# Optimization experiments

Measured on AMD Instinct MI355X. Metric: run time of the kernel, lower is better.

## Reference

```python
import jax, jax.numpy as jnp
import numpy as np

NUM_GRAPHS = 512


def setup_inputs() -> dict:
    key = jax.random.key(0)
    ks = jax.random.split(key, 12)
    N, E, D, H, C = 100000, 1600000, 128, 128, 10
    x = jax.random.normal(ks[0], (N, D), dtype=jnp.float32)
    edge_index = jax.random.randint(ks[1], (2, E), 0, N, dtype=jnp.int64)
    batch = jnp.sort(jax.random.randint(ks[2], (N,), 0, NUM_GRAPHS, dtype=jnp.int64))
    def glorot(k, fan_in, fan_out):
        s = jnp.sqrt(6.0 / (fan_in + fan_out))
        return jax.random.uniform(k, (fan_in, fan_out), jnp.float32, -s, s)
    return {
        "x": x, "edge_index": edge_index, "batch": batch,
        "W_init": glorot(ks[3], D, H), "b_init": jnp.zeros((H,), jnp.float32),
        "W_h0": glorot(ks[4], H, H), "b_h0": jnp.zeros((H,), jnp.float32),
        "W_h1": glorot(ks[5], H, H), "b_h1": jnp.zeros((H,), jnp.float32),
        "W_out": glorot(ks[6], H, C), "b_out": jnp.zeros((C,), jnp.float32),
    }


def reference(x, edge_index, batch, W_init, b_init, W_h0, b_h0, W_h1, b_h1, W_out, b_out):
    N = x.shape[0]
    loop = jnp.arange(N, dtype=edge_index.dtype)
    # add self-loops (PyG GCNConv default)
    row = jnp.concatenate([edge_index[0], loop])  # source
    col = jnp.concatenate([edge_index[1], loop])  # target
    # symmetric normalization D^-1/2 (A+I) D^-1/2, degrees on target index
    deg = jax.ops.segment_sum(jnp.ones_like(col, dtype=x.dtype), col, num_segments=N)
    dis = jnp.where(deg > 0, jax.lax.rsqrt(jnp.maximum(deg, 1e-12)), 0.0)
    norm = dis[row] * dis[col]  # [E+N]

    def gcn_conv(h, W, b):
        h = h @ W                                    # linear first (as in PyG)
        msg = h[row] * norm[:, None]                 # gather + scale
        return jax.ops.segment_sum(msg, col, num_segments=N) + b  # scatter-add

    h = jax.nn.relu(gcn_conv(x, W_init, b_init))
    h = jax.nn.relu(gcn_conv(h, W_h0, b_h0))
    h = jax.nn.relu(gcn_conv(h, W_h1, b_h1))
    h = gcn_conv(h, W_out, b_out)
    # global mean pooling over graphs
    sums = jax.ops.segment_sum(h, batch, num_segments=NUM_GRAPHS)
    cnt = jax.ops.segment_sum(jnp.ones((N, 1), h.dtype), batch, num_segments=NUM_GRAPHS)
    return sums / jnp.maximum(cnt, 1.0)
```

## Files before the change

### kernel.cpp

```cpp
#include <hip/hip_runtime.h>


#define SCAN_BLOCKS 64
#define SCAN_THREADS (SCAN_BLOCKS * 256)

typedef unsigned short u16;
typedef unsigned int   u32;
typedef __attribute__((ext_vector_type(8))) short bf16x8;
typedef __attribute__((ext_vector_type(4))) float f32x4;

static __device__ __forceinline__ u16 f2bf(float x) {
    u32 u = __float_as_uint(x);
    u32 r = (u + 0x7fffu + ((u >> 16) & 1u)) >> 16;
    return (u16)r;
}
static __device__ __forceinline__ float bf_lo(u32 p) { return __uint_as_float(p << 16); }
static __device__ __forceinline__ float bf_hi(u32 p) { return __uint_as_float(p & 0xffff0000u); }

__global__ __launch_bounds__(256) void k_count(const int* __restrict__ col, int E,
                                               int* __restrict__ cnt,
                                               u16* __restrict__ rank) {
    int e = blockIdx.x * 256 + threadIdx.x;
    if (e < E) rank[e] = (u16)atomicAdd(&cnt[col[e]], 1);
}

__global__ __launch_bounds__(256) void k_scan1(const int* __restrict__ cnt,
                                               int* __restrict__ tsum, int N) {
    int t = blockIdx.x * 256 + threadIdx.x;
    int strip = (N + SCAN_THREADS - 1) / SCAN_THREADS;
    int s0 = t * strip;
    int s1 = s0 + strip; if (s1 > N) s1 = N;
    int s = 0;
    for (int i = s0; i < s1; ++i) s += (cnt[i] + 3) & ~3;
    tsum[t] = s;
}

__global__ __launch_bounds__(1024) void k_scan2(int* __restrict__ tsum) {
    __shared__ int part[1024];
    int t = threadIdx.x;
    int base = t * 16;
    int local[16];
    int s = 0;
    #pragma unroll
    for (int i = 0; i < 16; ++i) { local[i] = tsum[base + i]; s += local[i]; }
    part[t] = s;
    __syncthreads();
    for (int off = 1; off < 1024; off <<= 1) {
        int v = part[t];
        int add = (t >= off) ? part[t - off] : 0;
        __syncthreads();
        part[t] = v + add;
        __syncthreads();
    }
    int run = (t == 0) ? 0 : part[t - 1];
    #pragma unroll
    for (int i = 0; i < 16; ++i) { int c = local[i]; tsum[base + i] = run; run += c; }
}

__global__ __launch_bounds__(256) void k_scan3(const int* __restrict__ cnt,
                                               const int* __restrict__ tsum,
                                               int* __restrict__ rowptr,
                                               float* __restrict__ dis,
                                               int* __restrict__ csr, int N) {
    int t = blockIdx.x * 256 + threadIdx.x;
    int strip = (N + SCAN_THREADS - 1) / SCAN_THREADS;
    int s0 = t * strip;
    int s1 = s0 + strip; if (s1 > N) s1 = N;
    int run = tsum[t];
    for (int i = s0; i < s1; ++i) {
        int c = cnt[i];
        int r = (c + 3) & ~3;
        rowptr[i] = run;
        for (int p = run + c; p < run + r; ++p) csr[p] = N;
        run += r;
        dis[i] = rsqrtf((float)(c + 1));
    }
    if (t == SCAN_THREADS - 1) rowptr[N] = run;
}

__global__ __launch_bounds__(256) void k_fill(const int* __restrict__ row,
                                              const int* __restrict__ col, int E,
                                              const int* __restrict__ rowptr,
                                              const u16* __restrict__ rank,
                                              int* __restrict__ csr) {
    int e = blockIdx.x * 256 + threadIdx.x;
    if (e < E) {
        int c = col[e];
        csr[rowptr[c] + (int)rank[e]] = row[e];
    }
}

__global__ __launch_bounds__(256) void k_cast(const float* __restrict__ src,
                                              const float* __restrict__ dis,
                                              u16* __restrict__ bX,
                                              u16* __restrict__ bA,
                                              u16* __restrict__ bB, int N) {
    int i = blockIdx.x * 256 + threadIdx.x;
    int total = (N + 1) * 32;
    if (i >= total) return;
    int v = i >> 5;
    if (v < N) {
        float dv = dis[v];
        float4 val = ((const float4*)src)[i];
        ushort4 o;
        o.x = f2bf(dv * val.x); o.y = f2bf(dv * val.y);
        o.z = f2bf(dv * val.z); o.w = f2bf(dv * val.w);
        ((ushort4*)bX)[i] = o;
    } else {
        ushort4 z = {0, 0, 0, 0};
        ((ushort4*)bX)[i] = z;
        ((ushort4*)bA)[i] = z;
        ((ushort4*)bB)[i] = z;
    }
}

__global__ __launch_bounds__(256) void k_wprep4(const float* __restrict__ W0,
                                                const float* __restrict__ W1,
                                                const float* __restrict__ W2,
                                                const float* __restrict__ Wo,
                                                u32* __restrict__ whi,
                                                u32* __restrict__ wlo, int C) {
    if (blockIdx.x < 24) {
        int which = blockIdx.x >> 3;
        const float* W = (which == 0) ? W0 : (which == 1) ? W1 : W2;
        int t = (blockIdx.x & 7) * 256 + threadIdx.x;
        int lane = t & 63;
        int nk = t >> 6;
        int k0 = nk & 3;
        int ntile = nk >> 2;
        int n = ntile * 16 + (lane & 15);
        int kbase = k0 * 32 + (lane >> 4) * 8;
        u32 hi[4], lo[4];
        #pragma unroll
        for (int tt = 0; tt < 4; ++tt) {
            float w0 = W[(kbase + 2 * tt) * 128 + n];
            float w1 = W[(kbase + 2 * tt + 1) * 128 + n];
            u16 h0 = f2bf(w0), h1 = f2bf(w1);
            u16 l0 = f2bf(w0 - __uint_as_float((u32)h0 << 16));
            u16 l1 = f2bf(w1 - __uint_as_float((u32)h1 << 16));
            hi[tt] = (u32)h0 | ((u32)h1 << 16);
            lo[tt] = (u32)l0 | ((u32)l1 << 16);
        }
        uint4 qh = {hi[0], hi[1], hi[2], hi[3]};
        uint4 ql = {lo[0], lo[1], lo[2], lo[3]};
        int base = which * 2048;
        ((uint4*)whi)[base + t] = qh;
        ((uint4*)wlo)[base + t] = ql;
    } else {
        int t = threadIdx.x;
        int lane = t & 63;
        int k0 = t >> 6;
        int n = lane & 15;
        int kbase = k0 * 32 + (lane >> 4) * 8;
        bool vc = (n < C);
        u32 hi[4], lo[4];
        #pragma unroll
        for (int tt = 0; tt < 4; ++tt) {
            float w0 = vc ? Wo[(kbase + 2 * tt) * C + n] : 0.f;
            float w1 = vc ? Wo[(kbase + 2 * tt + 1) * C + n] : 0.f;
            u16 h0 = f2bf(w0), h1 = f2bf(w1);
            u16 l0 = f2bf(w0 - __uint_as_float((u32)h0 << 16));
            u16 l1 = f2bf(w1 - __uint_as_float((u32)h1 << 16));
            hi[tt] = (u32)h0 | ((u32)h1 << 16);
            lo[tt] = (u32)l0 | ((u32)l1 << 16);
        }
        uint4 qh = {hi[0], hi[1], hi[2], hi[3]};
        uint4 ql = {lo[0], lo[1], lo[2], lo[3]};
        ((uint4*)whi)[6144 + t] = qh;
        ((uint4*)wlo)[6144 + t] = ql;
    }
}

__global__ __launch_bounds__(256) void k_fused(const u16* __restrict__ hin,
                                               const u32* __restrict__ whi,
                                               const u32* __restrict__ wlo,
                                               const float* __restrict__ bias,
                                               u16* __restrict__ hout,
                                               const int* __restrict__ rowptr,
                                               const int* __restrict__ csr,
                                               const float* __restrict__ dis,
                                               int N, int scale_out,
                                               int proj,
                                               const u32* __restrict__ pwhi,
                                               const u32* __restrict__ pwlo,
                                               float* __restrict__ tmpC) {
    __shared__ u32 sS[32 * 68];
    __shared__ float dS[32];
    int tid = threadIdx.x;
    int wave = tid >> 6;
    int lane = tid & 63;
    int row0 = blockIdx.x * 32;
    const u32* hin32 = (const u32*)hin;
    const int4* csr4 = (const int4*)csr;

    for (int j = 0; j < 8; j += 2) {
        int va = row0 + wave * 8 + j;
        int vb = va + 1;
        bool hA = va < N, hB = vb < N;
        float ax = 0.f, ay = 0.f, bx = 0.f, by = 0.f;
        int ia = 0, ea = 0, ib = 0, eb = 0;
        float dva = 1.f, dvb = 1.f;
        if (hA) {
            u32 p = hin32[((u32)va << 6) + lane];
            ax = bf_lo(p); ay = bf_hi(p);
            ia = rowptr[va]; ea = rowptr[va + 1];
            dva = dis[va];
        }
        if (hB) {
            u32 p = hin32[((u32)vb << 6) + lane];
            bx = bf_lo(p); by = bf_hi(p);
            ib = rowptr[vb]; eb = rowptr[vb + 1];
            dvb = dis[vb];
        }
        while ((ia + 8 <= ea) & (ib + 8 <= eb)) {
            int4 a0 = csr4[(u32)ia >> 2];
            int4 a1 = csr4[((u32)ia >> 2) + 1];
            int4 b0 = csr4[(u32)ib >> 2];
            int4 b1 = csr4[((u32)ib >> 2) + 1];
            u32 pa0 = hin32[((u32)a0.x << 6) + lane];
            u32 pa1 = hin32[((u32)a0.y << 6) + lane];
            u32 pa2 = hin32[((u32)a0.z << 6) + lane];
            u32 pa3 = hin32[((u32)a0.w << 6) + lane];
            u32 pa4 = hin32[((u32)a1.x << 6) + lane];
            u32 pa5 = hin32[((u32)a1.y << 6) + lane];
            u32 pa6 = hin32[((u32)a1.z << 6) + lane];
            u32 pa7 = hin32[((u32)a1.w << 6) + lane];
            u32 pb0 = hin32[((u32)b0.x << 6) + lane];
            u32 pb1 = hin32[((u32)b0.y << 6) + lane];
            u32 pb2 = hin32[((u32)b0.z << 6) + lane];
            u32 pb3 = hin32[((u32)b0.w << 6) + lane];
            u32 pb4 = hin32[((u32)b1.x << 6) + lane];
            u32 pb5 = hin32[((u32)b1.y << 6) + lane];
            u32 pb6 = hin32[((u32)b1.z << 6) + lane];
            u32 pb7 = hin32[((u32)b1.w << 6) + lane];
            ax += bf_lo(pa0) + bf_lo(pa1) + bf_lo(pa2) + bf_lo(pa3);
            ay += bf_hi(pa0) + bf_hi(pa1) + bf_hi(pa2) + bf_hi(pa3);
            ax += bf_lo(pa4) + bf_lo(pa5) + bf_lo(pa6) + bf_lo(pa7);
            ay += bf_hi(pa4) + bf_hi(pa5) + bf_hi(pa6) + bf_hi(pa7);
            bx += bf_lo(pb0) + bf_lo(pb1) + bf_lo(pb2) + bf_lo(pb3);
            by += bf_hi(pb0) + bf_hi(pb1) + bf_hi(pb2) + bf_hi(pb3);
            bx += bf_lo(pb4) + bf_lo(pb5) + bf_lo(pb6) + bf_lo(pb7);
            by += bf_hi(pb4) + bf_hi(pb5) + bf_hi(pb6) + bf_hi(pb7);
            ia += 8; ib += 8;
        }
        while (ia + 8 <= ea) {
            int4 a0 = csr4[(u32)ia >> 2];
            int4 a1 = csr4[((u32)ia >> 2) + 1];
            u32 p0 = hin32[((u32)a0.x << 6) + lane];
            u32 p1 = hin32[((u32)a0.y << 6) + lane];
            u32 p2 = hin32[((u32)a0.z << 6) + lane];
            u32 p3 = hin32[((u32)a0.w << 6) + lane];
            u32 p4 = hin32[((u32)a1.x << 6) + lane];
            u32 p5 = hin32[((u32)a1.y << 6) + lane];
            u32 p6 = hin32[((u32)a1.z << 6) + lane];
            u32 p7 = hin32[((u32)a1.w << 6) + lane];
            ax += bf_lo(p0) + bf_lo(p1) + bf_lo(p2) + bf_lo(p3);
            ay += bf_hi(p0) + bf_hi(p1) + bf_hi(p2) + bf_hi(p3);
            ax += bf_lo(p4) + bf_lo(p5) + bf_lo(p6) + bf_lo(p7);
            ay += bf_hi(p4) + bf_hi(p5) + bf_hi(p6) + bf_hi(p7);
            ia += 8;
        }
        if (ia < ea) {
            int4 a0 = csr4[(u32)ia >> 2];
            u32 p0 = hin32[((u32)a0.x << 6) + lane];
            u32 p1 = hin32[((u32)a0.y << 6) + lane];
            u32 p2 = hin32[((u32)a0.z << 6) + lane];
            u32 p3 = hin32[((u32)a0.w << 6) + lane];
            ax += bf_lo(p0) + bf_lo(p1) + bf_lo(p2) + bf_lo(p3);
            ay += bf_hi(p0) + bf_hi(p1) + bf_hi(p2) + bf_hi(p3);
        }
        while (ib + 8 <= eb) {
            int4 b0 = csr4[(u32)ib >> 2];
            int4 b1 = csr4[((u32)ib >> 2) + 1];
            u32 p0 = hin32[((u32)b0.x << 6) + lane];
            u32 p1 = hin32[((u32)b0.y << 6) + lane];
            u32 p2 = hin32[((u32)b0.z << 6) + lane];
            u32 p3 = hin32[((u32)b0.w << 6) + lane];
            u32 p4 = hin32[((u32)b1.x << 6) + lane];
            u32 p5 = hin32[((u32)b1.y << 6) + lane];
            u32 p6 = hin32[((u32)b1.z << 6) + lane];
            u32 p7 = hin32[((u32)b1.w << 6) + lane];
            bx += bf_lo(p0) + bf_lo(p1) + bf_lo(p2) + bf_lo(p3);
            by += bf_hi(p0) + bf_hi(p1) + bf_hi(p2) + bf_hi(p3);
            bx += bf_lo(p4) + bf_lo(p5) + bf_lo(p6) + bf_lo(p7);
            by += bf_hi(p4) + bf_hi(p5) + bf_hi(p6) + bf_hi(p7);
            ib += 8;
        }
        if (ib < eb) {
            int4 b0 = csr4[(u32)ib >> 2];
            u32 p0 = hin32[((u32)b0.x << 6) + lane];
            u32 p1 = hin32[((u32)b0.y << 6) + lane];
            u32 p2 = hin32[((u32)b0.z << 6) + lane];
            u32 p3 = hin32[((u32)b0.w << 6) + lane];
            bx += bf_lo(p0) + bf_lo(p1) + bf_lo(p2) + bf_lo(p3);
            by += bf_hi(p0) + bf_hi(p1) + bf_hi(p2) + bf_hi(p3);
        }
        if (hA) {
            sS[(wave * 8 + j) * 65 + lane] =
                (u32)f2bf(dva * ax) | ((u32)f2bf(dva * ay) << 16);
            if (lane == 0) dS[wave * 8 + j] = dva;
        }
        if (hB) {
            sS[(wave * 8 + j + 1) * 65 + lane] =
                (u32)f2bf(dvb * bx) | ((u32)f2bf(dvb * by) << 16);
            if (lane == 0) dS[wave * 8 + j + 1] = dvb;
        }
    }
    __syncthreads();

    f32x4 acc[2][2] = {{{0.f,0.f,0.f,0.f},{0.f,0.f,0.f,0.f}},
                       {{0.f,0.f,0.f,0.f},{0.f,0.f,0.f,0.f}}};
    int mA = lane & 15;
    int qA = lane >> 4;
    #pragma unroll
    for (int k0 = 0; k0 < 4; ++k0) {
        union { u32 u[4]; bf16x8 v; } A0, A1;
        int ub = k0 * 16 + qA * 4;
        #pragma unroll
        for (int tt = 0; tt < 4; ++tt) {
            A0.u[tt] = sS[mA * 65 + ub + tt];
            A1.u[tt] = sS[(mA + 16) * 65 + ub + tt];
        }
        #pragma unroll
        for (int ct = 0; ct < 2; ++ct) {
            int ntk = ((2 * wave + ct) * 4 + k0) * 64 + lane;
            union { uint4 q; bf16x8 v; } BH, BL;
            BH.q = ((const uint4*)whi)[ntk];
            BL.q = ((const uint4*)wlo)[ntk];
            acc[0][ct] = __builtin_amdgcn_mfma_f32_16x16x32_bf16(A0.v, BH.v, acc[0][ct], 0, 0, 0);
            acc[0][ct] = __builtin_amdgcn_mfma_f32_16x16x32_bf16(A0.v, BL.v, acc[0][ct], 0, 0, 0);
            acc[1][ct] = __builtin_amdgcn_mfma_f32_16x16x32_bf16(A1.v, BH.v, acc[1][ct], 0, 0, 0);
            acc[1][ct] = __builtin_amdgcn_mfma_f32_16x16x32_bf16(A1.v, BL.v, acc[1][ct], 0, 0, 0);
        }
    }

    if (!proj) {
        #pragma unroll
        for (int rt = 0; rt < 2; ++rt) {
            #pragma unroll
            for (int ct = 0; ct < 2; ++ct) {
                int col = (2 * wave + ct) * 16 + (lane & 15);
                float bb = bias[col];
                #pragma unroll
                for (int r = 0; r < 4; ++r) {
                    int rloc = rt * 16 + (lane >> 4) * 4 + r;
                    int row = row0 + rloc;
                    if (row < N) {
                        float o = fmaxf(acc[rt][ct][r] + bb, 0.f);
                        if (scale_out) o *= dS[rloc];
                        hout[((u32)row << 7) + col] = f2bf(o);
                    }
                }
            }
        }
    } else {
        __syncthreads();
        u16* hS16 = (u16*)sS;
        #pragma unroll
        for (int rt = 0; rt < 2; ++rt) {
            #pragma unroll
            for (int ct = 0; ct < 2; ++ct) {
                int col = (2 * wave + ct) * 16 + (lane & 15);
                float bb = bias[col];
                #pragma unroll
                for (int r = 0; r < 4; ++r) {
                    int rloc = rt * 16 + (lane >> 4) * 4 + r;
                    hS16[rloc * 136 + col] = f2bf(fmaxf(acc[rt][ct][r] + bb, 0.f));
                }
            }
        }
        __syncthreads();
        if (wave < 2) {
            int m = lane & 15;
            int quad = lane >> 4;
            f32x4 a2 = {0.f, 0.f, 0.f, 0.f};
            #pragma unroll
            for (int k0 = 0; k0 < 4; ++k0) {
                bf16x8 Afrag = *(bf16x8*)&hS16[(wave * 16 + m) * 136 + k0 * 32 + quad * 8];
                union { uint4 q; bf16x8 v; } BH, BL;
                BH.q = ((const uint4*)pwhi)[k0 * 64 + lane];
                BL.q = ((const uint4*)pwlo)[k0 * 64 + lane];
                a2 = __builtin_amdgcn_mfma_f32_16x16x32_bf16(Afrag, BH.v, a2, 0, 0, 0);
                a2 = __builtin_amdgcn_mfma_f32_16x16x32_bf16(Afrag, BL.v, a2, 0, 0, 0);
            }
            #pragma unroll
            for (int r = 0; r < 4; ++r) {
                int rloc = wave * 16 + quad * 4 + r;
                int row = row0 + rloc;
                if (row < N) tmpC[((u32)row << 4) + m] = a2[r] * dS[rloc];
            }
        }
        if (blockIdx.x == 0 && tid < 16) tmpC[((u32)N << 4) + tid] = 0.f;
    }
}

__global__ __launch_bounds__(256) void k_aggpool(const float* __restrict__ tp,
                                                 const int* __restrict__ rowptr,
                                                 const int* __restrict__ csr,
                                                 const float* __restrict__ dis,
                                                 const int* __restrict__ batch,
                                                 const float* __restrict__ bout,
                                                 float* __restrict__ out,
                                                 int N, int C) {
    __shared__ float red[256];
    int g = blockIdx.x;
    int tid = threadIdx.x;
    int c = tid & 15;
    int rg = tid >> 4;
    int lo = 0, hi = N;
    while (lo < hi) { int m = (lo + hi) >> 1; if (batch[m] < g) lo = m + 1; else hi = m; }
    int lb = lo;
    hi = N;
    while (lo < hi) { int m = (lo + hi) >> 1; if (batch[m] <= g) lo = m + 1; else hi = m; }
    int ub = lo;
    const int4* csr4 = (const int4*)csr;
    float pacc = 0.f;
    for (int v = lb + rg; v < ub; v += 16) {
        float acc = tp[((u32)v << 4) + c];
        int i = rowptr[v], e = rowptr[v + 1];
        for (; i + 8 <= e; i += 8) {
            int4 q0 = csr4[(u32)i >> 2];
            int4 q1 = csr4[((u32)i >> 2) + 1];
            acc += tp[((u32)q0.x << 4) + c] + tp[((u32)q0.y << 4) + c]
                 + tp[((u32)q0.z << 4) + c] + tp[((u32)q0.w << 4) + c]
                 + tp[((u32)q1.x << 4) + c] + tp[((u32)q1.y << 4) + c]
                 + tp[((u32)q1.z << 4) + c] + tp[((u32)q1.w << 4) + c];
        }
        if (i < e) {
            int4 q0 = csr4[(u32)i >> 2];
            acc += tp[((u32)q0.x << 4) + c] + tp[((u32)q0.y << 4) + c]
                 + tp[((u32)q0.z << 4) + c] + tp[((u32)q0.w << 4) + c];
        }
        pacc += dis[v] * acc;
    }
    red[tid] = pacc;
    __syncthreads();
    #pragma unroll
    for (int s = 8; s >= 1; s >>= 1) {
        if (rg < s) red[tid] += red[tid + s * 16];
        __syncthreads();
    }
    if (tid < C) {
        float cnt = (float)(ub - lb);
        out[g * C + tid] = (red[tid] + cnt * bout[tid]) / fmaxf(cnt, 1.0f);
    }
}

extern "C" void kernel_launch(void* const* d_in, const int* in_sizes, int n_in,
                              void* d_out, int out_size, void* d_ws, size_t ws_size,
                              hipStream_t stream) {
    const float* x      = (const float*)d_in[0];
    const int*   ei     = (const int*)d_in[1];
    const int*   batch  = (const int*)d_in[2];
    const float* W_init = (const float*)d_in[3];
    const float* b_init = (const float*)d_in[4];
    const float* W_h0   = (const float*)d_in[5];
    const float* b_h0   = (const float*)d_in[6];
    const float* W_h1   = (const float*)d_in[7];
    const float* b_h1   = (const float*)d_in[8];
    const float* W_out  = (const float*)d_in[9];
    const float* b_out  = (const float*)d_in[10];

    int N = in_sizes[0] / 128;
    int E = in_sizes[1] / 2;
    int C = in_sizes[10];
    int G = out_size / C;

    size_t off = 0;
    auto alloc = [&](size_t bytes) -> char* {
        char* p = (char*)d_ws + off;
        off += (bytes + 255) & ~(size_t)255;
        return p;
    };
    u16*   bufX   = (u16*)  alloc((size_t)(N + 1) * 128 * 2);
    u16*   bufA   = (u16*)  alloc((size_t)(N + 1) * 128 * 2);
    u16*   bufB   = (u16*)  alloc((size_t)(N + 1) * 128 * 2);
    float* dis    = (float*)alloc((size_t)N * 4);
    int*   rowptr = (int*)  alloc((size_t)(N + 1) * 4);
    int*   csr    = (int*)  alloc(((size_t)E + 3 * (size_t)N + 8) * 4);
    int*   tsum   = (int*)  alloc((size_t)SCAN_THREADS * 4);
    u32*   whi    = (u32*)  alloc((3 * 2048 + 256) * 16);
    u32*   wlo    = (u32*)  alloc((3 * 2048 + 256) * 16);
    size_t zoff   = off;
    int*   cnt    = (int*)  alloc((size_t)N * 4);
    size_t zbytes = off - zoff;

    u16*   rank   = (u16*)bufB;
    float* tmpC   = (float*)bufX;

    hipMemsetAsync(cnt, 0, zbytes, stream);

    const int* rowi = ei;
    const int* coli = ei + E;

    int eb = (E + 255) / 256;
    k_count<<<eb, 256, 0, stream>>>(coli, E, cnt, rank);
    k_scan1<<<SCAN_BLOCKS, 256, 0, stream>>>(cnt, tsum, N);
    k_scan2<<<1, 1024, 0, stream>>>(tsum);
    k_scan3<<<SCAN_BLOCKS, 256, 0, stream>>>(cnt, tsum, rowptr, dis, csr, N);
    k_fill<<<eb, 256, 0, stream>>>(rowi, coli, E, rowptr, rank, csr);

    k_wprep4<<<25, 256, 0, stream>>>(W_init, W_h0, W_h1, W_out, whi, wlo, C);

    int cg = ((N + 1) * 32 + 255) / 256;
    k_cast<<<cg, 256, 0, stream>>>(x, dis, bufX, bufA, bufB, N);

    int fb = (N + 31) / 32;

    k_fused<<<fb, 256, 0, stream>>>(bufX, whi,         wlo,         b_init, bufA, rowptr, csr, dis, N, 1, 0, nullptr, nullptr, nullptr);
    k_fused<<<fb, 256, 0, stream>>>(bufA, whi + 8192,  wlo + 8192,  b_h0,   bufB, rowptr, csr, dis, N, 1, 0, nullptr, nullptr, nullptr);
    k_fused<<<fb, 256, 0, stream>>>(bufB, whi + 16384, wlo + 16384, b_h1,   bufA, rowptr, csr, dis, N, 0, 1, whi + 24576, wlo + 24576, tmpC);

    k_aggpool<<<G, 256, 0, stream>>>(tmpC, rowptr, csr, dis, batch, b_out, (float*)d_out, N, C);
}
```

Baseline: 497.8 us.

## Gather neighbor rows with 16-lane groups using 16-byte loads per lane

The aggregation phase now has each wave process four rows at once: a 16-lane group covers one row, and each lane loads a uint4 holding 8 bf16 features. The old scheme spent the whole wave on two rows with 4-byte loads per lane. Loop trip counts are the maximum degree across the four groups, and out-of-range slots are padded by gathering row N, which relies on hin having a zero padding row at index N. The aim is fewer, wider memory transactions and more memory-level parallelism, at the cost of wasted gathers when degrees differ within a wave and of reading CSR entries past the end of a row's range.

```diff
diff --git a/kernel.cpp b/kernel.cpp
--- a/kernel.cpp
+++ b/kernel.cpp
@@ -190,121 +190,79 @@
     int wave = tid >> 6;
     int lane = tid & 63;
     int row0 = blockIdx.x * 32;
-    const u32* hin32 = (const u32*)hin;
-    const int4* csr4 = (const int4*)csr;
-
-    for (int j = 0; j < 8; j += 2) {
-        int va = row0 + wave * 8 + j;
-        int vb = va + 1;
-        bool hA = va < N, hB = vb < N;
-        float ax = 0.f, ay = 0.f, bx = 0.f, by = 0.f;
-        int ia = 0, ea = 0, ib = 0, eb = 0;
-        float dva = 1.f, dvb = 1.f;
-        if (hA) {
-            u32 p = hin32[((u32)va << 6) + lane];
-            ax = bf_lo(p); ay = bf_hi(p);
-            ia = rowptr[va]; ea = rowptr[va + 1];
-            dva = dis[va];
-        }
-        if (hB) {
-            u32 p = hin32[((u32)vb << 6) + lane];
-            bx = bf_lo(p); by = bf_hi(p);
-            ib = rowptr[vb]; eb = rowptr[vb + 1];
-            dvb = dis[vb];
-        }
-        while ((ia + 8 <= ea) & (ib + 8 <= eb)) {
-            int4 a0 = csr4[(u32)ia >> 2];
-            int4 a1 = csr4[((u32)ia >> 2) + 1];
-            int4 b0 = csr4[(u32)ib >> 2];
-            int4 b1 = csr4[((u32)ib >> 2) + 1];
-            u32 pa0 = hin32[((u32)a0.x << 6) + lane];
-            u32 pa1 = hin32[((u32)a0.y << 6) + lane];
-            u32 pa2 = hin32[((u32)a0.z << 6) + lane];
-            u32 pa3 = hin32[((u32)a0.w << 6) + lane];
-            u32 pa4 = hin32[((u32)a1.x << 6) + lane];
-            u32 pa5 = hin32[((u32)a1.y << 6) + lane];
-            u32 pa6 = hin32[((u32)a1.z << 6) + lane];
-            u32 pa7 = hin32[((u32)a1.w << 6) + lane];
-            u32 pb0 = hin32[((u32)b0.x << 6) + lane];
-            u32 pb1 = hin32[((u32)b0.y << 6) + lane];
-            u32 pb2 = hin32[((u32)b0.z << 6) + lane];
-            u32 pb3 = hin32[((u32)b0.w << 6) + lane];
-            u32 pb4 = hin32[((u32)b1.x << 6) + lane];
-            u32 pb5 = hin32[((u32)b1.y << 6) + lane];
-            u32 pb6 = hin32[((u32)b1.z << 6) + lane];
-            u32 pb7 = hin32[((u32)b1.w << 6) + lane];
-            ax += bf_lo(pa0) + bf_lo(pa1) + bf_lo(pa2) + bf_lo(pa3);
-            ay += bf_hi(pa0) + bf_hi(pa1) + bf_hi(pa2) + bf_hi(pa3);
-            ax += bf_lo(pa4) + bf_lo(pa5) + bf_lo(pa6) + bf_lo(pa7);
-            ay += bf_hi(pa4) + bf_hi(pa5) + bf_hi(pa6) + bf_hi(pa7);
-            bx += bf_lo(pb0) + bf_lo(pb1) + bf_lo(pb2) + bf_lo(pb3);
-            by += bf_hi(pb0) + bf_hi(pb1) + bf_hi(pb2) + bf_hi(pb3);
-            bx += bf_lo(pb4) + bf_lo(pb5) + bf_lo(pb6) + bf_lo(pb7);
-            by += bf_hi(pb4) + bf_hi(pb5) + bf_hi(pb6) + bf_hi(pb7);
-            ia += 8; ib += 8;
-        }
-        while (ia + 8 <= ea) {
-            int4 a0 = csr4[(u32)ia >> 2];
-            int4 a1 = csr4[((u32)ia >> 2) + 1];
-            u32 p0 = hin32[((u32)a0.x << 6) + lane];
-            u32 p1 = hin32[((u32)a0.y << 6) + lane];
-            u32 p2 = hin32[((u32)a0.z << 6) + lane];
-            u32 p3 = hin32[((u32)a0.w << 6) + lane];
-            u32 p4 = hin32[((u32)a1.x << 6) + lane];
-            u32 p5 = hin32[((u32)a1.y << 6) + lane];
-            u32 p6 = hin32[((u32)a1.z << 6) + lane];
-            u32 p7 = hin32[((u32)a1.w << 6) + lane];
-            ax += bf_lo(p0) + bf_lo(p1) + bf_lo(p2) + bf_lo(p3);
-            ay += bf_hi(p0) + bf_hi(p1) + bf_hi(p2) + bf_hi(p3);
-            ax += bf_lo(p4) + bf_lo(p5) + bf_lo(p6) + bf_lo(p7);
-            ay += bf_hi(p4) + bf_hi(p5) + bf_hi(p6) + bf_hi(p7);
-            ia += 8;
-        }
-        if (ia < ea) {
-            int4 a0 = csr4[(u32)ia >> 2];
-            u32 p0 = hin32[((u32)a0.x << 6) + lane];
-            u32 p1 = hin32[((u32)a0.y << 6) + lane];
-            u32 p2 = hin32[((u32)a0.z << 6) + lane];
-            u32 p3 = hin32[((u32)a0.w << 6) + lane];
-            ax += bf_lo(p0) + bf_lo(p1) + bf_lo(p2) + bf_lo(p3);
-            ay += bf_hi(p0) + bf_hi(p1) + bf_hi(p2) + bf_hi(p3);
-        }
-        while (ib + 8 <= eb) {
-            int4 b0 = csr4[(u32)ib >> 2];
-            int4 b1 = csr4[((u32)ib >> 2) + 1];
-            u32 p0 = hin32[((u32)b0.x << 6) + lane];
-            u32 p1 = hin32[((u32)b0.y << 6) + lane];
-            u32 p2 = hin32[((u32)b0.z << 6) + lane];
-            u32 p3 = hin32[((u32)b0.w << 6) + lane];
-            u32 p4 = hin32[((u32)b1.x << 6) + lane];
-            u32 p5 = hin32[((u32)b1.y << 6) + lane];
-            u32 p6 = hin32[((u32)b1.z << 6) + lane];
-            u32 p7 = hin32[((u32)b1.w << 6) + lane];
-            bx += bf_lo(p0) + bf_lo(p1) + bf_lo(p2) + bf_lo(p3);
-            by += bf_hi(p0) + bf_hi(p1) + bf_hi(p2) + bf_hi(p3);
-            bx += bf_lo(p4) + bf_lo(p5) + bf_lo(p6) + bf_lo(p7);
-            by += bf_hi(p4) + bf_hi(p5) + bf_hi(p6) + bf_hi(p7);
-            ib += 8;
-        }
-        if (ib < eb) {
-            int4 b0 = csr4[(u32)ib >> 2];
-            u32 p0 = hin32[((u32)b0.x << 6) + lane];
-            u32 p1 = hin32[((u32)b0.y << 6) + lane];
-            u32 p2 = hin32[((u32)b0.z << 6) + lane];
-            u32 p3 = hin32[((u32)b0.w << 6) + lane];
-            bx += bf_lo(p0) + bf_lo(p1) + bf_lo(p2) + bf_lo(p3);
-            by += bf_hi(p0) + bf_hi(p1) + bf_hi(p2) + bf_hi(p3);
-        }
-        if (hA) {
-            sS[(wave * 8 + j) * 65 + lane] =
-                (u32)f2bf(dva * ax) | ((u32)f2bf(dva * ay) << 16);
-            if (lane == 0) dS[wave * 8 + j] = dva;
-        }
-        if (hB) {
-            sS[(wave * 8 + j + 1) * 65 + lane] =
-                (u32)f2bf(dvb * bx) | ((u32)f2bf(dvb * by) << 16);
-            if (lane == 0) dS[wave * 8 + j + 1] = dvb;
-        }
+    const uint4* hin4 = (const uint4*)hin;
+
+    int grp = lane >> 4;
+    int sub = lane & 15;
+    #pragma unroll
+    for (int jj = 0; jj < 2; ++jj) {
+        int rloc = wave * 8 + jj * 4 + grp;
+        int row = row0 + rloc;
+        bool hR = row < N;
+        int ia = 0, rem = 0;
+        float dv = 1.f;
+        if (hR) {
+            ia  = rowptr[row];
+            rem = rowptr[row + 1] - ia;
+            dv  = dis[row];
+        }
+        int nself = hR ? row : N;
+        uint4 ps = hin4[((u32)nself << 4) + sub];
+        float a0 = bf_lo(ps.x), a1 = bf_hi(ps.x);
+        float a2 = bf_lo(ps.y), a3 = bf_hi(ps.y);
+        float a4 = bf_lo(ps.z), a5 = bf_hi(ps.z);
+        float a6 = bf_lo(ps.w), a7 = bf_hi(ps.w);
+        int m = rem;
+        m = max(m, __shfl_xor(m, 16));
+        m = max(m, __shfl_xor(m, 32));
+        const int4* cq = (const int4*)(csr + ia);
+        for (int k = 0; k < m; k += 8) {
+            int4 q0 = cq[(k >> 2)];
+            int4 q1 = cq[(k >> 2) + 1];
+            bool v0 = k < rem;
+            bool v1 = (k + 4) < rem;
+            int n0 = v0 ? q0.x : N;
+            int n1 = v0 ? q0.y : N;
+            int n2 = v0 ? q0.z : N;
+            int n3 = v0 ? q0.w : N;
+            int n4 = v1 ? q1.x : N;
+            int n5 = v1 ? q1.y : N;
+            int n6 = v1 ? q1.z : N;
+            int n7 = v1 ? q1.w : N;
+            uint4 p0 = hin4[((u32)n0 << 4) + sub];
+            uint4 p1 = hin4[((u32)n1 << 4) + sub];
+            uint4 p2 = hin4[((u32)n2 << 4) + sub];
+            uint4 p3 = hin4[((u32)n3 << 4) + sub];
+            uint4 p4 = hin4[((u32)n4 << 4) + sub];
+            uint4 p5 = hin4[((u32)n5 << 4) + sub];
+            uint4 p6 = hin4[((u32)n6 << 4) + sub];
+            uint4 p7 = hin4[((u32)n7 << 4) + sub];
+            a0 += bf_lo(p0.x) + bf_lo(p1.x) + bf_lo(p2.x) + bf_lo(p3.x);
+            a1 += bf_hi(p0.x) + bf_hi(p1.x) + bf_hi(p2.x) + bf_hi(p3.x);
+            a2 += bf_lo(p0.y) + bf_lo(p1.y) + bf_lo(p2.y) + bf_lo(p3.y);
+            a3 += bf_hi(p0.y) + bf_hi(p1.y) + bf_hi(p2.y) + bf_hi(p3.y);
+            a4 += bf_lo(p0.z) + bf_lo(p1.z) + bf_lo(p2.z) + bf_lo(p3.z);
+            a5 += bf_hi(p0.z) + bf_hi(p1.z) + bf_hi(p2.z) + bf_hi(p3.z);
+            a6 += bf_lo(p0.w) + bf_lo(p1.w) + bf_lo(p2.w) + bf_lo(p3.w);
+            a7 += bf_hi(p0.w) + bf_hi(p1.w) + bf_hi(p2.w) + bf_hi(p3.w);
+            a0 += bf_lo(p4.x) + bf_lo(p5.x) + bf_lo(p6.x) + bf_lo(p7.x);
+            a1 += bf_hi(p4.x) + bf_hi(p5.x) + bf_hi(p6.x) + bf_hi(p7.x);
+            a2 += bf_lo(p4.y) + bf_lo(p5.y) + bf_lo(p6.y) + bf_lo(p7.y);
+            a3 += bf_hi(p4.y) + bf_hi(p5.y) + bf_hi(p6.y) + bf_hi(p7.y);
+            a4 += bf_lo(p4.z) + bf_lo(p5.z) + bf_lo(p6.z) + bf_lo(p7.z);
+            a5 += bf_hi(p4.z) + bf_hi(p5.z) + bf_hi(p6.z) + bf_hi(p7.z);
+            a6 += bf_lo(p4.w) + bf_lo(p5.w) + bf_lo(p6.w) + bf_lo(p7.w);
+            a7 += bf_hi(p4.w) + bf_hi(p5.w) + bf_hi(p6.w) + bf_hi(p7.w);
+        }
+        u32 w0 = (u32)f2bf(dv * a0) | ((u32)f2bf(dv * a1) << 16);
+        u32 w1 = (u32)f2bf(dv * a2) | ((u32)f2bf(dv * a3) << 16);
+        u32 w2 = (u32)f2bf(dv * a4) | ((u32)f2bf(dv * a5) << 16);
+        u32 w3 = (u32)f2bf(dv * a6) | ((u32)f2bf(dv * a7) << 16);
+        sS[rloc * 65 + sub * 4 + 0] = w0;
+        sS[rloc * 65 + sub * 4 + 1] = w1;
+        sS[rloc * 65 + sub * 4 + 2] = w2;
+        sS[rloc * 65 + sub * 4 + 3] = w3;
+        if (sub == 0) dS[rloc] = dv;
     }
     __syncthreads();
 
@@ -371,12 +329,12 @@
         }
         __syncthreads();
         if (wave < 2) {
-            int m = lane & 15;
+            int m2 = lane & 15;
             int quad = lane >> 4;
             f32x4 a2 = {0.f, 0.f, 0.f, 0.f};
             #pragma unroll
             for (int k0 = 0; k0 < 4; ++k0) {
-                bf16x8 Afrag = *(bf16x8*)&hS16[(wave * 16 + m) * 136 + k0 * 32 + quad * 8];
+                bf16x8 Afrag = *(bf16x8*)&hS16[(wave * 16 + m2) * 136 + k0 * 32 + quad * 8];
                 union { uint4 q; bf16x8 v; } BH, BL;
                 BH.q = ((const uint4*)pwhi)[k0 * 64 + lane];
                 BL.q = ((const uint4*)pwlo)[k0 * 64 + lane];
@@ -387,7 +345,7 @@
             for (int r = 0; r < 4; ++r) {
                 int rloc = wave * 16 + quad * 4 + r;
                 int row = row0 + rloc;
-                if (row < N) tmpC[((u32)row << 4) + m] = a2[r] * dS[rloc];
+                if (row < N) tmpC[((u32)row << 4) + m2] = a2[r] * dS[rloc];
             }
         }
         if (blockIdx.x == 0 && tid < 16) tmpC[((u32)N << 4) + tid] = 0.f;
```

Measured after the change: 468.0 us. 6.0% less time.
